# Kernel tuning notes

Hardware: AMD Instinct MI355X
Metric: run time of the kernel (lower is better)

Reference implementation:

```python
import jax, jax.numpy as jnp
import numpy as np

B, T, C = 2, 192, 512
H, D = 8, 64  # num_heads, head_dim; inner_dim = H*D = C


def setup_inputs() -> dict:
    key = jax.random.key(0)
    k1, k2, k3 = jax.random.split(key, 3)
    x = jax.random.normal(k1, (B, T, C), dtype=jnp.float32)
    W_in = jax.random.normal(k2, (C, 5 * H * D), dtype=jnp.float32) * 0.02
    b_in = jnp.zeros((5 * H * D,), dtype=jnp.float32)
    W_out = jax.random.normal(k3, (H * D, C), dtype=jnp.float32) * 0.02
    b_out = jnp.zeros((C,), dtype=jnp.float32)
    return {"x": x, "W_in": W_in, "b_in": b_in, "W_out": W_out, "b_out": b_out}


def _split_heads(t):
    # (B,T,H*D) -> (B,H,T,D)
    return t.reshape(B, T, H, D).transpose(0, 2, 1, 3)


def reference(x, W_in, b_in, W_out, b_out):
    scale = D ** -0.5
    proj = x @ W_in + b_in  # (B,T,5*H*D)
    q, k1, v1, k2, v2 = jnp.split(proj, 5, axis=-1)
    q = _split_heads(q) * scale
    k1 = _split_heads(k1)
    v1 = _split_heads(v1)
    k2 = _split_heads(k2)
    v2 = _split_heads(v2)
    # trilinear logits: <q_i, k1_j, k2_k> / sqrt(D), computed in fp32
    logits = jnp.einsum('bhid,bhjd,bhkd->bhijk', q, k1, k2,
                        preferred_element_type=jnp.float32)
    # softmax over the joint (j,k) axes
    attn = jax.nn.softmax(logits.reshape(B, H, T, T * T), axis=-1)
    attn = attn.reshape(B, H, T, T, T).astype(x.dtype)
    # out_i[d] = sum_{j,k} attn[i,j,k] * v1_j[d] * v2_k[d]
    out = jnp.einsum('bhijk,bhjd,bhkd->bhid', attn, v1, v2)
    y = out.transpose(0, 2, 1, 3).reshape(B, T, H * D)  # merge heads
    return y @ W_out + b_out
```

## Files before the change

kernel.cpp:

```cpp
#include <hip/hip_runtime.h>
#include <hip/hip_bf16.h>


typedef float  v4f __attribute__((ext_vector_type(4)));
typedef short  v8s __attribute__((ext_vector_type(8)));

__device__ __forceinline__ unsigned short f2bf(float f) {
  unsigned u = __float_as_uint(f);
  u += 0x7fffu + ((u >> 16) & 1u);
  return (unsigned short)(u >> 16);
}
__device__ __forceinline__ float bf2f(unsigned short b) {
  return __uint_as_float(((unsigned)b) << 16);
}
__device__ __forceinline__ unsigned pack_bf16(float lo, float hi) {
  __hip_bfloat162 t = __float22bfloat162_rn(float2{lo, hi});
  union { __hip_bfloat162 b; unsigned u; } cv;
  cv.b = t;
  return cv.u;
}

#if __has_builtin(__builtin_amdgcn_exp2f)
#define EXP2F(x) __builtin_amdgcn_exp2f(x)
#else
#define EXP2F(x) exp2f(x)
#endif

#define MFMA32(a, b, c) __builtin_amdgcn_mfma_f32_16x16x32_bf16((a), (b), (c), 0, 0, 0)

#define QSCALE 0.18033688011112042f


#define XH_OFF   589824
#define XL_OFF   786432
#define WTH_OFF  983040
#define WTL_OFF  2293760
#define WOTH_OFF 3604480
#define WOTL_OFF 3866624
#define OH_OFF   4128768
#define OL_OFF   4325376

__device__ __forceinline__ int v1perm(int t) {
  return (t & ~31) | (((t >> 2) & 3) << 3) | ((t & 3) << 1) | ((t >> 4) & 1);
}

__global__ __launch_bounds__(256) void prep_kernel(
    const float* __restrict__ x, const float* __restrict__ Win,
    const float* __restrict__ Wout, unsigned short* __restrict__ wsh) {
  __shared__ float tile[32 * 65];
  const int bi = blockIdx.x, t = threadIdx.x;
  if (bi < 768) {
    const float* W; unsigned short *Th, *Tl; int R, n0, k0;
    if (bi < 640) {
      W = Win; Th = wsh + WTH_OFF; Tl = wsh + WTL_OFF; R = 2560;
      n0 = (bi % 40) << 6; k0 = (bi / 40) << 5;
    } else {
      const int idx = bi - 640;
      W = Wout; Th = wsh + WOTH_OFF; Tl = wsh + WOTL_OFF; R = 512;
      n0 = (idx & 7) << 6; k0 = (idx >> 3) << 5;
    }
    const int n = t & 63, kq = (t >> 6) * 8;
#pragma unroll
    for (int j = 0; j < 8; ++j)
      tile[(kq + j) * 65 + n] = W[(k0 + kq + j) * R + n0 + n];
    __syncthreads();
    const int n2 = t >> 2, ks = (t & 3) * 8;
    union { uint4 u; unsigned short us[8]; } ph, pl;
#pragma unroll
    for (int j = 0; j < 8; ++j) {
      const float v = tile[(ks + j) * 65 + n2];
      const unsigned short h = f2bf(v);
      ph.us[j] = h;
      pl.us[j] = f2bf(v - bf2f(h));
    }
    *(uint4*)(Th + (n0 + n2) * 512 + k0 + ks) = ph.u;
    *(uint4*)(Tl + (n0 + n2) * 512 + k0 + ks) = pl.u;
  } else {
    const int flat = ((bi - 768) * 256 + t) * 8;
    const v4f v0 = *(const v4f*)(x + flat);
    const v4f v1 = *(const v4f*)(x + flat + 4);
    union { uint4 u; unsigned short us[8]; } ph, pl;
#pragma unroll
    for (int j = 0; j < 4; ++j) {
      unsigned short h = f2bf(v0[j]);
      ph.us[j] = h; pl.us[j] = f2bf(v0[j] - bf2f(h));
      h = f2bf(v1[j]);
      ph.us[4 + j] = h; pl.us[4 + j] = f2bf(v1[j] - bf2f(h));
    }
    *(uint4*)(wsh + XH_OFF + flat) = ph.u;
    *(uint4*)(wsh + XL_OFF + flat) = pl.u;
  }
}

__global__ __launch_bounds__(64) void proj_kernel(
    const unsigned short* __restrict__ wsh, const float* __restrict__ bin,
    float* __restrict__ wsf, unsigned short* __restrict__ wshd) {
  const int lane = threadIdx.x;
  const int c = lane & 15, q = lane >> 4;
  const int bm = blockIdx.x % 12, bn = blockIdx.x / 12;

  const unsigned short* base[8];
  base[0] = wsh + XH_OFF + (bm * 32 + c) * 512 + (q << 3);
  base[1] = base[0] + 16 * 512;
  base[2] = wsh + XL_OFF + (bm * 32 + c) * 512 + (q << 3);
  base[3] = base[2] + 16 * 512;
  base[4] = wsh + WTH_OFF + (bn * 32 + c) * 512 + (q << 3);
  base[5] = base[4] + 16 * 512;
  base[6] = wsh + WTL_OFF + (bn * 32 + c) * 512 + (q << 3);
  base[7] = base[6] + 16 * 512;

  const v4f z = {0.f, 0.f, 0.f, 0.f};
  v4f a00 = z, a01 = z, a10 = z, a11 = z;

  v8s cur[8], nxt[8];
#pragma unroll
  for (int i = 0; i < 8; ++i) cur[i] = *(const v8s*)(base[i]);
#pragma unroll
  for (int i = 0; i < 8; ++i) nxt[i] = *(const v8s*)(base[i] + 32);

#pragma unroll 1
  for (int ks = 0; ks < 16; ++ks) {
    v8s nx2[8];
    if (ks < 14) {
      const int o = (ks + 2) * 32;
#pragma unroll
      for (int i = 0; i < 8; ++i) nx2[i] = *(const v8s*)(base[i] + o);
    }
    a00 = MFMA32(cur[2], cur[4], a00); a00 = MFMA32(cur[0], cur[6], a00); a00 = MFMA32(cur[0], cur[4], a00);
    a01 = MFMA32(cur[2], cur[5], a01); a01 = MFMA32(cur[0], cur[7], a01); a01 = MFMA32(cur[0], cur[5], a01);
    a10 = MFMA32(cur[3], cur[4], a10); a10 = MFMA32(cur[1], cur[6], a10); a10 = MFMA32(cur[1], cur[4], a10);
    a11 = MFMA32(cur[3], cur[5], a11); a11 = MFMA32(cur[1], cur[7], a11); a11 = MFMA32(cur[1], cur[5], a11);
#pragma unroll
    for (int i = 0; i < 8; ++i) { cur[i] = nxt[i]; nxt[i] = nx2[i]; }
  }

  v4f accs[2][2] = {{a00, a01}, {a10, a11}};
#pragma unroll
  for (int mt = 0; mt < 2; ++mt) {
#pragma unroll
    for (int nt = 0; nt < 2; ++nt) {
      const int n = bn * 32 + nt * 16 + c;
      const int which = n >> 9, cc = n & 511, h = cc >> 6, d = cc & 63;
      const float bv = bin[n];
#pragma unroll
      for (int r = 0; r < 4; ++r) {
        const int m = bm * 32 + mt * 16 + (q << 2) + r;
        const int b = (m >= 192) ? 1 : 0;
        const int tt = m - (b ? 192 : 0);
        const int bh = b * 8 + h;
        const float val = accs[mt][nt][r] + bv;
        const int rm = ((bh * 192 + tt) << 6) + d;
        if (which == 0)      wsf[rm] = val * QSCALE;
        else if (which == 1) wshd[rm] = f2bf(val);
        else if (which == 2) wshd[393216 + ((bh << 6) + d) * 192 + v1perm(tt)] = f2bf(val);
        else if (which == 3) wshd[196608 + rm] = f2bf(val);
        else wsf[196608 + ((bh * 192 + tt) * 16 + (d & 15)) * 4 + (d >> 4)] = val;
      }
    }
  }
}

__global__ __launch_bounds__(256, 2) void attn_kernel(
    const float* __restrict__ wsf, const unsigned short* __restrict__ wsh,
    float* __restrict__ accp, float* __restrict__ Sp) {
  __shared__ char smem[58368];
  unsigned short* V1s = (unsigned short*)smem;
  unsigned short* K2s = (unsigned short*)(smem + 25600);

  const int tid  = threadIdx.x;
  const int wv   = tid >> 6;
  const int lane = tid & 63;
  const int c    = lane & 15;
  const int quad = lane >> 4;

  const int bb = blockIdx.x;
  const int kb = bb & 3;
  const int it = (bb >> 2) % 12;
  const int bh = bb / 48;

  const unsigned short* k1g = wsh + bh * 192 * 64;
  const unsigned short* v1g = wsh + 393216 + bh * 64 * 192;
  const unsigned short* k2g = wsh + 196608 + bh * 192 * 64;
  const float*          v2g = wsf + 196608 + bh * 12288;

  for (int idx = tid; idx < 1920; idx += 256) {
    if (idx < 1536) {
      const int r = idx / 24, c8 = (idx % 24) * 8;
      *(uint4*)(V1s + r * 200 + c8) = *(const uint4*)(v1g + r * 192 + c8);
    } else {
      const int j = idx - 1536;
      const int r = j >> 3, c8 = (j & 7) * 8;
      *(uint4*)(K2s + r * 64 + c8) = *(const uint4*)(k2g + (kb * 48 + r) * 64 + c8);
    }
  }

  v8s k1f[12][2];
#pragma unroll
  for (int jt = 0; jt < 12; ++jt) {
    const unsigned short* kp = k1g + ((jt * 16 + c) << 6) + (quad << 3);
    k1f[jt][0] = *(const v8s*)(kp);
    k1f[jt][1] = *(const v8s*)(kp + 32);
  }

  const float* qg = wsf + ((bh * 192 + it * 16 + c) << 6) + (quad << 3);
  float q0[8], q1[8];
  {
    v4f qa = *(const v4f*)(qg), qb = *(const v4f*)(qg + 4);
    v4f qc = *(const v4f*)(qg + 32), qd = *(const v4f*)(qg + 36);
#pragma unroll
    for (int e = 0; e < 4; ++e) {
      q0[e] = qa[e]; q0[4 + e] = qb[e];
      q1[e] = qc[e]; q1[4 + e] = qd[e];
    }
  }
  __syncthreads();

  unsigned* Pw = (unsigned*)(smem + 31744) + wv * 1664;
  const v4f z = {0.f, 0.f, 0.f, 0.f};
  v4f acc[4] = {z, z, z, z};
  v4f oSA = z, oSB = z;
  const short one = (short)0x3F80;
  const v8s ones = {one, one, one, one, one, one, one, one};

  const int kloc0 = wv * 12;
  union U4 { uint4 u4; unsigned short us[8]; };
  union AF { v8s v; unsigned u[4]; };

#pragma unroll 1
  for (int p = 0; p < 6; ++p) {
    const int rA = kloc0 + 2 * p, rB = rA + 1;
    U4 klA, khA, klB, khB;
    klA.u4 = *(const uint4*)(K2s + rA * 64 + (quad << 3));
    khA.u4 = *(const uint4*)(K2s + rA * 64 + (quad << 3) + 32);
    klB.u4 = *(const uint4*)(K2s + rB * 64 + (quad << 3));
    khB.u4 = *(const uint4*)(K2s + rB * 64 + (quad << 3) + 32);
    const v4f v2A = *(const v4f*)(v2g + (((kb * 48 + rA) << 4) + c) * 4);
    const v4f v2B = *(const v4f*)(v2g + (((kb * 48 + rB) << 4) + c) * 4);

    AF af[2][2];
#pragma unroll
    for (int e = 0; e < 4; ++e) {
      af[0][0].u[e] = pack_bf16(q0[2*e] * bf2f(klA.us[2*e]), q0[2*e+1] * bf2f(klA.us[2*e+1]));
      af[0][1].u[e] = pack_bf16(q1[2*e] * bf2f(khA.us[2*e]), q1[2*e+1] * bf2f(khA.us[2*e+1]));
      af[1][0].u[e] = pack_bf16(q0[2*e] * bf2f(klB.us[2*e]), q0[2*e+1] * bf2f(klB.us[2*e+1]));
      af[1][1].u[e] = pack_bf16(q1[2*e] * bf2f(khB.us[2*e]), q1[2*e+1] * bf2f(khB.us[2*e+1]));
    }

    v4f oA[4] = {z, z, z, z}, oB[4] = {z, z, z, z};

#pragma unroll
    for (int h = 0; h < 2; ++h) {
#pragma unroll
      for (int kk = 0; kk < 2; ++kk) {
        v4f C[6];
#pragma unroll
        for (int jj = 0; jj < 6; ++jj) {
          const int jt = h * 6 + jj;
          v4f t0 = MFMA32(af[kk][0].v, k1f[jt][0], z);
          C[jj] = MFMA32(af[kk][1].v, k1f[jt][1], t0);
        }
#pragma unroll
        for (int jj = 0; jj < 6; ++jj)
#pragma unroll
          for (int r = 0; r < 4; ++r) C[jj][r] = EXP2F(C[jj][r]);
#pragma unroll
        for (int m = 0; m < 3; ++m)
#pragma unroll
          for (int r = 0; r < 4; ++r)
            Pw[kk * 832 + ((quad << 2) + r) * 52 + m * 16 + c] =
                pack_bf16(C[2*m][r], C[2*m+1][r]);
      }
#pragma unroll
      for (int m = 0; m < 3; ++m) {
        const v8s apA = *(const v8s*)(Pw + c * 52 + m * 16 + (quad << 2));
        const v8s apB = *(const v8s*)(Pw + 832 + c * 52 + m * 16 + (quad << 2));
        oSA = MFMA32(apA, ones, oSA);
        oSB = MFMA32(apB, ones, oSB);
        const int vcol = (h * 3 + m) * 32 + (quad << 3);
#pragma unroll
        for (int t = 0; t < 4; ++t) {
          const v8s vf = *(const v8s*)(V1s + (c + 16 * t) * 200 + vcol);
          oA[t] = MFMA32(apA, vf, oA[t]);
          oB[t] = MFMA32(apB, vf, oB[t]);
        }
      }
    }
#pragma unroll
    for (int t = 0; t < 4; ++t) acc[t] += oA[t] * v2A[t] + oB[t] * v2B[t];
  }

  __syncthreads();
  float* redA = (float*)smem;
  float* redS = (float*)smem + 4096;

  if (c == 0) {
    float* rs = redS + wv * 16 + (quad << 2);
#pragma unroll
    for (int r = 0; r < 4; ++r) rs[r] = oSA[r] + oSB[r];
  }
#pragma unroll
  for (int r = 0; r < 4; ++r) {
    float* rr = redA + wv * 1024 + (((quad << 2) + r) << 6) + c;
    rr[0] = acc[0][r]; rr[16] = acc[1][r]; rr[32] = acc[2][r]; rr[48] = acc[3][r];
  }
  __syncthreads();

  const int pbase = (bh * 12 + it) * 4 + kb;
  float* ap_out = accp + pbase * 1024;
  for (int idx = tid; idx < 1024; idx += 256)
    ap_out[idx] = redA[idx] + redA[1024 + idx] + redA[2048 + idx] + redA[3072 + idx];
  if (tid < 16)
    Sp[pbase * 16 + tid] = redS[tid] + redS[16 + tid] + redS[32 + tid] + redS[48 + tid];
}

__global__ __launch_bounds__(256) void norm_kernel(
    const float* __restrict__ accp, const float* __restrict__ Sp,
    unsigned short* __restrict__ wsh) {
  const int flat = blockIdx.x * 2048 + threadIdx.x * 8;
  const int m = flat >> 9, cc = flat & 511;
  const int b = (m >= 192) ? 1 : 0;
  const int tt = m - (b ? 192 : 0);
  const int h = cc >> 6, d0 = cc & 63;
  const int bh = b * 8 + h, it = tt >> 4, i = tt & 15;
  const int pb = (bh * 12 + it) * 4;
  const float* ap = accp + pb * 1024 + (i << 6) + d0;
  v4f a0 = *(const v4f*)(ap), a1 = *(const v4f*)(ap + 4);
  float Sv = Sp[pb * 16 + i];
#pragma unroll
  for (int kb = 1; kb < 4; ++kb) {
    a0 += *(const v4f*)(ap + kb * 1024);
    a1 += *(const v4f*)(ap + kb * 1024 + 4);
    Sv += Sp[(pb + kb) * 16 + i];
  }
  const float inv = 1.0f / Sv;
  union { uint4 u; unsigned short us[8]; } ph, pl;
#pragma unroll
  for (int j = 0; j < 4; ++j) {
    float v = a0[j] * inv;
    unsigned short hh = f2bf(v);
    ph.us[j] = hh; pl.us[j] = f2bf(v - bf2f(hh));
    v = a1[j] * inv;
    hh = f2bf(v);
    ph.us[4 + j] = hh; pl.us[4 + j] = f2bf(v - bf2f(hh));
  }
  *(uint4*)(wsh + OH_OFF + flat) = ph.u;
  *(uint4*)(wsh + OL_OFF + flat) = pl.u;
}

__global__ __launch_bounds__(64) void outp_kernel(
    const unsigned short* __restrict__ wsh, const float* __restrict__ bout,
    float* __restrict__ y) {
  const int lane = threadIdx.x;
  const int c = lane & 15, q = lane >> 4;
  const int bm = blockIdx.x % 12, bn = blockIdx.x / 12;

  const unsigned short* base[8];
  base[0] = wsh + OH_OFF + (bm * 32 + c) * 512 + (q << 3);
  base[1] = base[0] + 16 * 512;
  base[2] = wsh + OL_OFF + (bm * 32 + c) * 512 + (q << 3);
  base[3] = base[2] + 16 * 512;
  base[4] = wsh + WOTH_OFF + (bn * 32 + c) * 512 + (q << 3);
  base[5] = base[4] + 16 * 512;
  base[6] = wsh + WOTL_OFF + (bn * 32 + c) * 512 + (q << 3);
  base[7] = base[6] + 16 * 512;

  const v4f z = {0.f, 0.f, 0.f, 0.f};
  v4f a00 = z, a01 = z, a10 = z, a11 = z;

  v8s cur[8], nxt[8];
#pragma unroll
  for (int i = 0; i < 8; ++i) cur[i] = *(const v8s*)(base[i]);
#pragma unroll
  for (int i = 0; i < 8; ++i) nxt[i] = *(const v8s*)(base[i] + 32);

#pragma unroll 1
  for (int ks = 0; ks < 16; ++ks) {
    v8s nx2[8];
    if (ks < 14) {
      const int o = (ks + 2) * 32;
#pragma unroll
      for (int i = 0; i < 8; ++i) nx2[i] = *(const v8s*)(base[i] + o);
    }
    a00 = MFMA32(cur[2], cur[4], a00); a00 = MFMA32(cur[0], cur[6], a00); a00 = MFMA32(cur[0], cur[4], a00);
    a01 = MFMA32(cur[2], cur[5], a01); a01 = MFMA32(cur[0], cur[7], a01); a01 = MFMA32(cur[0], cur[5], a01);
    a10 = MFMA32(cur[3], cur[4], a10); a10 = MFMA32(cur[1], cur[6], a10); a10 = MFMA32(cur[1], cur[4], a10);
    a11 = MFMA32(cur[3], cur[5], a11); a11 = MFMA32(cur[1], cur[7], a11); a11 = MFMA32(cur[1], cur[5], a11);
#pragma unroll
    for (int i = 0; i < 8; ++i) { cur[i] = nxt[i]; nxt[i] = nx2[i]; }
  }

  v4f accs[2][2] = {{a00, a01}, {a10, a11}};
#pragma unroll
  for (int mt = 0; mt < 2; ++mt) {
#pragma unroll
    for (int nt = 0; nt < 2; ++nt) {
      const int n = bn * 32 + nt * 16 + c;
      const float bv = bout[n];
#pragma unroll
      for (int r = 0; r < 4; ++r) {
        const int m = bm * 32 + mt * 16 + (q << 2) + r;
        y[m * 512 + n] = accs[mt][nt][r] + bv;
      }
    }
  }
}

extern "C" void kernel_launch(void* const* d_in, const int* in_sizes, int n_in,
                              void* d_out, int out_size, void* d_ws, size_t ws_size,
                              hipStream_t stream) {
  const float* x    = (const float*)d_in[0];
  const float* Win  = (const float*)d_in[1];
  const float* bin  = (const float*)d_in[2];
  const float* Wout = (const float*)d_in[3];
  const float* bout = (const float*)d_in[4];

  float* wsf = (float*)d_ws;
  unsigned short* wsh = (unsigned short*)(wsf + 1191936);
  float* accp = wsf + 393216;
  float* Sp   = wsf + 1179648;

  prep_kernel<<<dim3(864), 256, 0, stream>>>(x, Win, Wout, wsh);
  proj_kernel<<<dim3(960), 64, 0, stream>>>(wsh, bin, wsf, wsh);
  attn_kernel<<<dim3(768), 256, 0, stream>>>(wsf, wsh, accp, Sp);
  norm_kernel<<<dim3(96), 256, 0, stream>>>(accp, Sp, wsh);
  outp_kernel<<<dim3(192), 64, 0, stream>>>(wsh, bout, (float*)d_out);
}
```

Baseline: 145.1 us.

## Split-K projection GEMMs across waves and keep attention probabilities in registers

The projection and output GEMMs now use 256-thread blocks where four waves each take a quarter of K, and the partial tiles are summed through shared memory. The attention kernel drops the LDS staging of probabilities: the operand order of the logit MFMA is swapped so the exp'd tile can be packed straight into A-fragments, with v1perm updated to match. K1 moves from registers into LDS, K2 and V2 are read from global memory, and occupancy is raised to 3 blocks per CU. This aims to cut register pressure and LDS round-trips, at the cost of more global reads and a reduction step in the GEMMs.

```diff
diff --git a/kernel.cpp b/kernel.cpp
--- a/kernel.cpp
+++ b/kernel.cpp
@@ -41,7 +41,13 @@
 #define OL_OFF   4325376
 
 __device__ __forceinline__ int v1perm(int t) {
-  return (t & ~31) | (((t >> 2) & 3) << 3) | ((t & 3) << 1) | ((t >> 4) & 1);
+  const int h = (t >= 96) ? 1 : 0;
+  const int jh = t - 96 * h;
+  const int jtl = jh >> 4, rem = jh & 15;
+  const int m = jtl >> 1;
+  const int w = ((jtl & 1) << 1) | ((rem >> 1) & 1);
+  const int k = ((rem >> 2) << 3) | (w << 1) | (rem & 1);
+  return h * 96 + m * 32 + k;
 }
 
 __global__ __launch_bounds__(256) void prep_kernel(
@@ -92,21 +98,24 @@
   }
 }
 
-__global__ __launch_bounds__(64) void proj_kernel(
+__global__ __launch_bounds__(256) void proj_kernel(
     const unsigned short* __restrict__ wsh, const float* __restrict__ bin,
     float* __restrict__ wsf, unsigned short* __restrict__ wshd) {
-  const int lane = threadIdx.x;
+  __shared__ float red[4][32][33];
+  const int tid = threadIdx.x;
+  const int wv = tid >> 6, lane = tid & 63;
   const int c = lane & 15, q = lane >> 4;
-  const int bm = blockIdx.x % 12, bn = blockIdx.x / 12;
+  const int bm = blockIdx.x, bn = blockIdx.y;
+  const int k0 = wv * 128;
 
   const unsigned short* base[8];
-  base[0] = wsh + XH_OFF + (bm * 32 + c) * 512 + (q << 3);
+  base[0] = wsh + XH_OFF + (bm * 32 + c) * 512 + (q << 3) + k0;
   base[1] = base[0] + 16 * 512;
-  base[2] = wsh + XL_OFF + (bm * 32 + c) * 512 + (q << 3);
+  base[2] = wsh + XL_OFF + (bm * 32 + c) * 512 + (q << 3) + k0;
   base[3] = base[2] + 16 * 512;
-  base[4] = wsh + WTH_OFF + (bn * 32 + c) * 512 + (q << 3);
+  base[4] = wsh + WTH_OFF + (bn * 32 + c) * 512 + (q << 3) + k0;
   base[5] = base[4] + 16 * 512;
-  base[6] = wsh + WTL_OFF + (bn * 32 + c) * 512 + (q << 3);
+  base[6] = wsh + WTL_OFF + (bn * 32 + c) * 512 + (q << 3) + k0;
   base[7] = base[6] + 16 * 512;
 
   const v4f z = {0.f, 0.f, 0.f, 0.f};
@@ -115,57 +124,58 @@
   v8s cur[8], nxt[8];
 #pragma unroll
   for (int i = 0; i < 8; ++i) cur[i] = *(const v8s*)(base[i]);
-#pragma unroll
-  for (int i = 0; i < 8; ++i) nxt[i] = *(const v8s*)(base[i] + 32);
-
 #pragma unroll 1
-  for (int ks = 0; ks < 16; ++ks) {
-    v8s nx2[8];
-    if (ks < 14) {
-      const int o = (ks + 2) * 32;
-#pragma unroll
-      for (int i = 0; i < 8; ++i) nx2[i] = *(const v8s*)(base[i] + o);
+  for (int ks = 0; ks < 4; ++ks) {
+    if (ks < 3) {
+      const int o = (ks + 1) * 32;
+#pragma unroll
+      for (int i = 0; i < 8; ++i) nxt[i] = *(const v8s*)(base[i] + o);
     }
     a00 = MFMA32(cur[2], cur[4], a00); a00 = MFMA32(cur[0], cur[6], a00); a00 = MFMA32(cur[0], cur[4], a00);
     a01 = MFMA32(cur[2], cur[5], a01); a01 = MFMA32(cur[0], cur[7], a01); a01 = MFMA32(cur[0], cur[5], a01);
     a10 = MFMA32(cur[3], cur[4], a10); a10 = MFMA32(cur[1], cur[6], a10); a10 = MFMA32(cur[1], cur[4], a10);
     a11 = MFMA32(cur[3], cur[5], a11); a11 = MFMA32(cur[1], cur[7], a11); a11 = MFMA32(cur[1], cur[5], a11);
 #pragma unroll
-    for (int i = 0; i < 8; ++i) { cur[i] = nxt[i]; nxt[i] = nx2[i]; }
+    for (int i = 0; i < 8; ++i) cur[i] = nxt[i];
   }
 
   v4f accs[2][2] = {{a00, a01}, {a10, a11}};
 #pragma unroll
-  for (int mt = 0; mt < 2; ++mt) {
-#pragma unroll
-    for (int nt = 0; nt < 2; ++nt) {
-      const int n = bn * 32 + nt * 16 + c;
-      const int which = n >> 9, cc = n & 511, h = cc >> 6, d = cc & 63;
-      const float bv = bin[n];
-#pragma unroll
-      for (int r = 0; r < 4; ++r) {
-        const int m = bm * 32 + mt * 16 + (q << 2) + r;
-        const int b = (m >= 192) ? 1 : 0;
-        const int tt = m - (b ? 192 : 0);
-        const int bh = b * 8 + h;
-        const float val = accs[mt][nt][r] + bv;
-        const int rm = ((bh * 192 + tt) << 6) + d;
-        if (which == 0)      wsf[rm] = val * QSCALE;
-        else if (which == 1) wshd[rm] = f2bf(val);
-        else if (which == 2) wshd[393216 + ((bh << 6) + d) * 192 + v1perm(tt)] = f2bf(val);
-        else if (which == 3) wshd[196608 + rm] = f2bf(val);
-        else wsf[196608 + ((bh * 192 + tt) * 16 + (d & 15)) * 4 + (d >> 4)] = val;
-      }
-    }
-  }
-}
-
-__global__ __launch_bounds__(256, 2) void attn_kernel(
+  for (int mt = 0; mt < 2; ++mt)
+#pragma unroll
+    for (int nt = 0; nt < 2; ++nt)
+#pragma unroll
+      for (int r = 0; r < 4; ++r)
+        red[wv][mt * 16 + (q << 2) + r][nt * 16 + c] = accs[mt][nt][r];
+  __syncthreads();
+
+#pragma unroll
+  for (int j = 0; j < 4; ++j) {
+    const int o = tid + (j << 8);
+    const int row = o >> 5, col = o & 31;
+    const int n = bn * 32 + col;
+    const float val = red[0][row][col] + red[1][row][col] +
+                      red[2][row][col] + red[3][row][col] + bin[n];
+    const int m = bm * 32 + row;
+    const int which = n >> 9, cc = n & 511, hh = cc >> 6, d = cc & 63;
+    const int b = (m >= 192) ? 1 : 0;
+    const int tt = m - (b ? 192 : 0);
+    const int bh = b * 8 + hh;
+    const int rm = ((bh * 192 + tt) << 6) + d;
+    if (which == 0)      wsf[rm] = val * QSCALE;
+    else if (which == 1) wshd[rm] = f2bf(val);
+    else if (which == 2) wshd[393216 + ((bh << 6) + d) * 192 + v1perm(tt)] = f2bf(val);
+    else if (which == 3) wshd[196608 + rm] = f2bf(val);
+    else wsf[196608 + ((bh * 192 + tt) * 16 + (d & 15)) * 4 + (d >> 4)] = val;
+  }
+}
+
+__global__ __launch_bounds__(256, 3) void attn_kernel(
     const float* __restrict__ wsf, const unsigned short* __restrict__ wsh,
     float* __restrict__ accp, float* __restrict__ Sp) {
-  __shared__ char smem[58368];
-  unsigned short* V1s = (unsigned short*)smem;
-  unsigned short* K2s = (unsigned short*)(smem + 25600);
+  __shared__ unsigned short smem[25600];
+  unsigned short* V1s = smem;
+  unsigned short* K1s = smem + 12544;
 
   const int tid  = threadIdx.x;
   const int wv   = tid >> 6;
@@ -183,23 +193,15 @@
   const unsigned short* k2g = wsh + 196608 + bh * 192 * 64;
   const float*          v2g = wsf + 196608 + bh * 12288;
 
-  for (int idx = tid; idx < 1920; idx += 256) {
+  for (int idx = tid; idx < 3072; idx += 256) {
     if (idx < 1536) {
       const int r = idx / 24, c8 = (idx % 24) * 8;
-      *(uint4*)(V1s + r * 200 + c8) = *(const uint4*)(v1g + r * 192 + c8);
+      *(uint4*)(V1s + r * 196 + c8) = *(const uint4*)(v1g + r * 192 + c8);
     } else {
       const int j = idx - 1536;
-      const int r = j >> 3, c8 = (j & 7) * 8;
-      *(uint4*)(K2s + r * 64 + c8) = *(const uint4*)(k2g + (kb * 48 + r) * 64 + c8);
-    }
-  }
-
-  v8s k1f[12][2];
-#pragma unroll
-  for (int jt = 0; jt < 12; ++jt) {
-    const unsigned short* kp = k1g + ((jt * 16 + c) << 6) + (quad << 3);
-    k1f[jt][0] = *(const v8s*)(kp);
-    k1f[jt][1] = *(const v8s*)(kp + 32);
+      const int r = j >> 3, c8 = (j & 7) << 3;
+      *(uint4*)(K1s + r * 68 + c8) = *(const uint4*)(k1g + (r << 6) + c8);
+    }
   }
 
   const float* qg = wsf + ((bh * 192 + it * 16 + c) << 6) + (quad << 3);
@@ -215,78 +217,81 @@
   }
   __syncthreads();
 
-  unsigned* Pw = (unsigned*)(smem + 31744) + wv * 1664;
   const v4f z = {0.f, 0.f, 0.f, 0.f};
   v4f acc[4] = {z, z, z, z};
-  v4f oSA = z, oSB = z;
+  v4f oS = z;
   const short one = (short)0x3F80;
   const v8s ones = {one, one, one, one, one, one, one, one};
 
-  const int kloc0 = wv * 12;
+  const int kstart = kb * 48 + wv * 12;
   union U4 { uint4 u4; unsigned short us[8]; };
   union AF { v8s v; unsigned u[4]; };
 
 #pragma unroll 1
   for (int p = 0; p < 6; ++p) {
-    const int rA = kloc0 + 2 * p, rB = rA + 1;
+    const int rA = kstart + 2 * p, rB = rA + 1;
     U4 klA, khA, klB, khB;
-    klA.u4 = *(const uint4*)(K2s + rA * 64 + (quad << 3));
-    khA.u4 = *(const uint4*)(K2s + rA * 64 + (quad << 3) + 32);
-    klB.u4 = *(const uint4*)(K2s + rB * 64 + (quad << 3));
-    khB.u4 = *(const uint4*)(K2s + rB * 64 + (quad << 3) + 32);
-    const v4f v2A = *(const v4f*)(v2g + (((kb * 48 + rA) << 4) + c) * 4);
-    const v4f v2B = *(const v4f*)(v2g + (((kb * 48 + rB) << 4) + c) * 4);
-
-    AF af[2][2];
+    klA.u4 = *(const uint4*)(k2g + (rA << 6) + (quad << 3));
+    khA.u4 = *(const uint4*)(k2g + (rA << 6) + (quad << 3) + 32);
+    klB.u4 = *(const uint4*)(k2g + (rB << 6) + (quad << 3));
+    khB.u4 = *(const uint4*)(k2g + (rB << 6) + (quad << 3) + 32);
+    const v4f v2A = *(const v4f*)(v2g + (rA << 6) + (c << 2));
+    const v4f v2B = *(const v4f*)(v2g + (rB << 6) + (c << 2));
+
+    AF afA0, afA1, afB0, afB1;
 #pragma unroll
     for (int e = 0; e < 4; ++e) {
-      af[0][0].u[e] = pack_bf16(q0[2*e] * bf2f(klA.us[2*e]), q0[2*e+1] * bf2f(klA.us[2*e+1]));
-      af[0][1].u[e] = pack_bf16(q1[2*e] * bf2f(khA.us[2*e]), q1[2*e+1] * bf2f(khA.us[2*e+1]));
-      af[1][0].u[e] = pack_bf16(q0[2*e] * bf2f(klB.us[2*e]), q0[2*e+1] * bf2f(klB.us[2*e+1]));
-      af[1][1].u[e] = pack_bf16(q1[2*e] * bf2f(khB.us[2*e]), q1[2*e+1] * bf2f(khB.us[2*e+1]));
-    }
-
-    v4f oA[4] = {z, z, z, z}, oB[4] = {z, z, z, z};
+      afA0.u[e] = pack_bf16(q0[2*e] * bf2f(klA.us[2*e]), q0[2*e+1] * bf2f(klA.us[2*e+1]));
+      afA1.u[e] = pack_bf16(q1[2*e] * bf2f(khA.us[2*e]), q1[2*e+1] * bf2f(khA.us[2*e+1]));
+      afB0.u[e] = pack_bf16(q0[2*e] * bf2f(klB.us[2*e]), q0[2*e+1] * bf2f(klB.us[2*e+1]));
+      afB1.u[e] = pack_bf16(q1[2*e] * bf2f(khB.us[2*e]), q1[2*e+1] * bf2f(khB.us[2*e+1]));
+    }
 
 #pragma unroll
     for (int h = 0; h < 2; ++h) {
-#pragma unroll
-      for (int kk = 0; kk < 2; ++kk) {
-        v4f C[6];
-#pragma unroll
-        for (int jj = 0; jj < 6; ++jj) {
-          const int jt = h * 6 + jj;
-          v4f t0 = MFMA32(af[kk][0].v, k1f[jt][0], z);
-          C[jj] = MFMA32(af[kk][1].v, k1f[jt][1], t0);
+      v4f CA[6], CB[6];
+#pragma unroll
+      for (int j6 = 0; j6 < 6; ++j6) {
+        const unsigned short* kp = K1s + ((h * 6 + j6) * 16 + c) * 68 + (quad << 3);
+        const v8s k1lo = *(const v8s*)kp;
+        const v8s k1hi = *(const v8s*)(kp + 32);
+        v4f t0 = MFMA32(k1lo, afA0.v, z);
+        CA[j6] = MFMA32(k1hi, afA1.v, t0);
+        v4f t1 = MFMA32(k1lo, afB0.v, z);
+        CB[j6] = MFMA32(k1hi, afB1.v, t1);
+      }
+#pragma unroll
+      for (int j6 = 0; j6 < 6; ++j6)
+#pragma unroll
+        for (int r = 0; r < 4; ++r) {
+          CA[j6][r] = EXP2F(CA[j6][r]);
+          CB[j6][r] = EXP2F(CB[j6][r]);
         }
-#pragma unroll
-        for (int jj = 0; jj < 6; ++jj)
-#pragma unroll
-          for (int r = 0; r < 4; ++r) C[jj][r] = EXP2F(C[jj][r]);
-#pragma unroll
-        for (int m = 0; m < 3; ++m)
-#pragma unroll
-          for (int r = 0; r < 4; ++r)
-            Pw[kk * 832 + ((quad << 2) + r) * 52 + m * 16 + c] =
-                pack_bf16(C[2*m][r], C[2*m+1][r]);
-      }
+      AF pA[3], pB[3];
+#pragma unroll
+      for (int m = 0; m < 3; ++m)
+#pragma unroll
+        for (int w = 0; w < 4; ++w) {
+          const int jt = 2 * m + (w >> 1), r0 = (w & 1) * 2;
+          pA[m].u[w] = pack_bf16(CA[jt][r0], CA[jt][r0 + 1]);
+          pB[m].u[w] = pack_bf16(CB[jt][r0], CB[jt][r0 + 1]);
+        }
+      v4f oA[4] = {z, z, z, z}, oB[4] = {z, z, z, z};
 #pragma unroll
       for (int m = 0; m < 3; ++m) {
-        const v8s apA = *(const v8s*)(Pw + c * 52 + m * 16 + (quad << 2));
-        const v8s apB = *(const v8s*)(Pw + 832 + c * 52 + m * 16 + (quad << 2));
-        oSA = MFMA32(apA, ones, oSA);
-        oSB = MFMA32(apB, ones, oSB);
+        oS = MFMA32(pA[m].v, ones, oS);
+        oS = MFMA32(pB[m].v, ones, oS);
         const int vcol = (h * 3 + m) * 32 + (quad << 3);
 #pragma unroll
         for (int t = 0; t < 4; ++t) {
-          const v8s vf = *(const v8s*)(V1s + (c + 16 * t) * 200 + vcol);
-          oA[t] = MFMA32(apA, vf, oA[t]);
-          oB[t] = MFMA32(apB, vf, oB[t]);
+          const v8s vf = *(const v8s*)(V1s + (c + 16 * t) * 196 + vcol);
+          oA[t] = MFMA32(pA[m].v, vf, oA[t]);
+          oB[t] = MFMA32(pB[m].v, vf, oB[t]);
         }
       }
-    }
-#pragma unroll
-    for (int t = 0; t < 4; ++t) acc[t] += oA[t] * v2A[t] + oB[t] * v2B[t];
+#pragma unroll
+      for (int t = 0; t < 4; ++t) acc[t] += oA[t] * v2A[t] + oB[t] * v2B[t];
+    }
   }
 
   __syncthreads();
@@ -296,7 +301,7 @@
   if (c == 0) {
     float* rs = redS + wv * 16 + (quad << 2);
 #pragma unroll
-    for (int r = 0; r < 4; ++r) rs[r] = oSA[r] + oSB[r];
+    for (int r = 0; r < 4; ++r) rs[r] = oS[r];
   }
 #pragma unroll
   for (int r = 0; r < 4; ++r) {
@@ -347,21 +352,24 @@
   *(uint4*)(wsh + OL_OFF + flat) = pl.u;
 }
 
-__global__ __launch_bounds__(64) void outp_kernel(
+__global__ __launch_bounds__(256) void outp_kernel(
     const unsigned short* __restrict__ wsh, const float* __restrict__ bout,
     float* __restrict__ y) {
-  const int lane = threadIdx.x;
+  __shared__ float red[4][32][33];
+  const int tid = threadIdx.x;
+  const int wv = tid >> 6, lane = tid & 63;
   const int c = lane & 15, q = lane >> 4;
-  const int bm = blockIdx.x % 12, bn = blockIdx.x / 12;
+  const int bm = blockIdx.x, bn = blockIdx.y;
+  const int k0 = wv * 128;
 
   const unsigned short* base[8];
-  base[0] = wsh + OH_OFF + (bm * 32 + c) * 512 + (q << 3);
+  base[0] = wsh + OH_OFF + (bm * 32 + c) * 512 + (q << 3) + k0;
   base[1] = base[0] + 16 * 512;
-  base[2] = wsh + OL_OFF + (bm * 32 + c) * 512 + (q << 3);
+  base[2] = wsh + OL_OFF + (bm * 32 + c) * 512 + (q << 3) + k0;
   base[3] = base[2] + 16 * 512;
-  base[4] = wsh + WOTH_OFF + (bn * 32 + c) * 512 + (q << 3);
+  base[4] = wsh + WOTH_OFF + (bn * 32 + c) * 512 + (q << 3) + k0;
   base[5] = base[4] + 16 * 512;
-  base[6] = wsh + WOTL_OFF + (bn * 32 + c) * 512 + (q << 3);
+  base[6] = wsh + WOTL_OFF + (bn * 32 + c) * 512 + (q << 3) + k0;
   base[7] = base[6] + 16 * 512;
 
   const v4f z = {0.f, 0.f, 0.f, 0.f};
@@ -370,38 +378,39 @@
   v8s cur[8], nxt[8];
 #pragma unroll
   for (int i = 0; i < 8; ++i) cur[i] = *(const v8s*)(base[i]);
-#pragma unroll
-  for (int i = 0; i < 8; ++i) nxt[i] = *(const v8s*)(base[i] + 32);
-
 #pragma unroll 1
-  for (int ks = 0; ks < 16; ++ks) {
-    v8s nx2[8];
-    if (ks < 14) {
-      const int o = (ks + 2) * 32;
-#pragma unroll
-      for (int i = 0; i < 8; ++i) nx2[i] = *(const v8s*)(base[i] + o);
+  for (int ks = 0; ks < 4; ++ks) {
+    if (ks < 3) {
+      const int o = (ks + 1) * 32;
+#pragma unroll
+      for (int i = 0; i < 8; ++i) nxt[i] = *(const v8s*)(base[i] + o);
     }
     a00 = MFMA32(cur[2], cur[4], a00); a00 = MFMA32(cur[0], cur[6], a00); a00 = MFMA32(cur[0], cur[4], a00);
     a01 = MFMA32(cur[2], cur[5], a01); a01 = MFMA32(cur[0], cur[7], a01); a01 = MFMA32(cur[0], cur[5], a01);
     a10 = MFMA32(cur[3], cur[4], a10); a10 = MFMA32(cur[1], cur[6], a10); a10 = MFMA32(cur[1], cur[4], a10);
     a11 = MFMA32(cur[3], cur[5], a11); a11 = MFMA32(cur[1], cur[7], a11); a11 = MFMA32(cur[1], cur[5], a11);
 #pragma unroll
-    for (int i = 0; i < 8; ++i) { cur[i] = nxt[i]; nxt[i] = nx2[i]; }
+    for (int i = 0; i < 8; ++i) cur[i] = nxt[i];
   }
 
   v4f accs[2][2] = {{a00, a01}, {a10, a11}};
 #pragma unroll
-  for (int mt = 0; mt < 2; ++mt) {
-#pragma unroll
-    for (int nt = 0; nt < 2; ++nt) {
-      const int n = bn * 32 + nt * 16 + c;
-      const float bv = bout[n];
-#pragma unroll
-      for (int r = 0; r < 4; ++r) {
-        const int m = bm * 32 + mt * 16 + (q << 2) + r;
-        y[m * 512 + n] = accs[mt][nt][r] + bv;
-      }
-    }
+  for (int mt = 0; mt < 2; ++mt)
+#pragma unroll
+    for (int nt = 0; nt < 2; ++nt)
+#pragma unroll
+      for (int r = 0; r < 4; ++r)
+        red[wv][mt * 16 + (q << 2) + r][nt * 16 + c] = accs[mt][nt][r];
+  __syncthreads();
+
+#pragma unroll
+  for (int j = 0; j < 4; ++j) {
+    const int o = tid + (j << 8);
+    const int row = o >> 5, col = o & 31;
+    const int n = bn * 32 + col;
+    const float val = red[0][row][col] + red[1][row][col] +
+                      red[2][row][col] + red[3][row][col] + bout[n];
+    y[(bm * 32 + row) * 512 + n] = val;
   }
 }
 
@@ -420,8 +429,8 @@
   float* Sp   = wsf + 1179648;
 
   prep_kernel<<<dim3(864), 256, 0, stream>>>(x, Win, Wout, wsh);
-  proj_kernel<<<dim3(960), 64, 0, stream>>>(wsh, bin, wsf, wsh);
+  proj_kernel<<<dim3(12, 80), 256, 0, stream>>>(wsh, bin, wsf, wsh);
   attn_kernel<<<dim3(768), 256, 0, stream>>>(wsf, wsh, accp, Sp);
   norm_kernel<<<dim3(96), 256, 0, stream>>>(accp, Sp, wsh);
-  outp_kernel<<<dim3(192), 64, 0, stream>>>(wsh, bout, (float*)d_out);
-}
+  outp_kernel<<<dim3(12, 16), 256, 0, stream>>>(wsh, bout, (float*)d_out);
+}
```

Result: slower. 224.2 us (+54.5%).
